# Optimization experiments

Hardware: AMD Instinct MI355X
Metric: run time of the kernel (lower is better)

The kernel has to match this reference:

```python
import jax, jax.numpy as jnp
import numpy as np

B, N, C, H = 32, 577, 768, 12
D = C // H  # head dim 64
HID = 3072  # hardcoded Mlp hidden
ALPHA = 0.1
EPS = 1e-6


def setup_inputs() -> dict:
    key = jax.random.key(0)
    ks = jax.random.split(key, 8)
    s = 0.02
    return {
        "x": jax.random.normal(ks[0], (B, N, C), jnp.float32),
        "attn_weight": jax.random.uniform(ks[1], (B, N - 1), jnp.float32),
        "ln1_w": jnp.ones((C,), jnp.float32),
        "ln1_b": jnp.zeros((C,), jnp.float32),
        "qkv_w": jax.random.normal(ks[2], (3 * C, C), jnp.float32) * s,
        "qkv_b": jnp.zeros((3 * C,), jnp.float32),
        "proj_w": jax.random.normal(ks[3], (C, C), jnp.float32) * s,
        "proj_b": jnp.zeros((C,), jnp.float32),
        "ln2_w": jnp.ones((C,), jnp.float32),
        "ln2_b": jnp.zeros((C,), jnp.float32),
        "fc1_w": jax.random.normal(ks[4], (HID, C), jnp.float32) * s,
        "fc1_b": jnp.zeros((HID,), jnp.float32),
        "fc2_w": jax.random.normal(ks[5], (C, HID), jnp.float32) * s,
        "fc2_b": jnp.zeros((C,), jnp.float32),
    }


def _ln(x, w, b):
    m = x.mean(-1, keepdims=True)
    v = jnp.var(x, axis=-1, keepdims=True)
    return (x - m) * jax.lax.rsqrt(v + EPS) * w + b


def reference(x, attn_weight, ln1_w, ln1_b, qkv_w, qkv_b, proj_w, proj_b,
              ln2_w, ln2_b, fc1_w, fc1_b, fc2_w, fc2_b):
    h = _ln(x, ln1_w, ln1_b)
    qkv = (h @ qkv_w.T + qkv_b).reshape(B, N, 3, H, D)
    q = qkv[:, :, 0].transpose(0, 2, 1, 3)  # [B,H,N,D]
    k = qkv[:, :, 1].transpose(0, 2, 1, 3)
    v = qkv[:, :, 2].transpose(0, 2, 1, 3)
    scale = D ** -0.5
    attn = jnp.einsum('bhnd,bhmd->bhnm', q, k) * scale  # [B,H,N,N]
    patch_attn = attn[:, :, 0, 1:]  # pre-reweight CLS->patch scores
    # multiplicative reweighting of CLS row (cols 1:) before softmax
    factor = jnp.concatenate(
        [jnp.ones((B, 1), attn.dtype), attn_weight * ALPHA + (1.0 - ALPHA)], axis=-1)
    attn = attn.at[:, :, 0, :].multiply(factor[:, None, :])
    attn = jax.nn.softmax(attn, axis=-1)
    out = jnp.einsum('bhnm,bhmd->bhnd', attn, v)
    out = out.transpose(0, 2, 1, 3).reshape(B, N, C)
    out = out @ proj_w.T + proj_b
    x = x + out
    h2 = _ln(x, ln2_w, ln2_b)
    h2 = jax.nn.gelu(h2 @ fc1_w.T + fc1_b, approximate=False)  # nn.GELU exact
    h2 = h2 @ fc2_w.T + fc2_b
    x = x + h2
    return (x, patch_attn)
```

## Files before the change

### kernel.cpp

```cpp
#include <hip/hip_runtime.h>
#include <hip/hip_bf16.h>
#include <cstdint>

#define BB 32
#define NN 577
#define CC 768
#define HH 12
#define HIDN 3072
#define MROWS (BB*NN)

typedef __attribute__((ext_vector_type(8))) short bf16x8;
typedef __attribute__((ext_vector_type(4))) float f32x4;

__device__ __forceinline__ float b2f(unsigned short u) {
    union { float f; unsigned int i; } x; x.i = ((unsigned int)u) << 16; return x.f;
}
__device__ __forceinline__ unsigned short f2b(float f) {
    union { float f; unsigned int i; } x; x.f = f;
    unsigned int i = x.i;
    i += 0x7fffu + ((i >> 16) & 1u);
    return (unsigned short)(i >> 16);
}

__device__ __forceinline__ void async16(const void* g, void* l) {
    __builtin_amdgcn_global_load_lds(
        (const __attribute__((address_space(1))) uint32_t*)g,
        (__attribute__((address_space(3))) uint32_t*)l, 16, 0, 0);
}

__device__ __forceinline__ float gelu_f(float v) {
    float ax = fabsf(v) * 0.70710678118654752f;
    float t = __builtin_amdgcn_rcpf(1.0f + 0.3275911f * ax);
    float poly = t * (0.254829592f + t * (-0.284496736f + t * (1.421413741f +
                 t * (-1.453152027f + t * 1.061405429f))));
    float e = __expf(-ax * ax);
    float erf_abs = 1.0f - poly * e;
    float erf_v = (v >= 0.f) ? erf_abs : -erf_abs;
    return 0.5f * v * (1.0f + erf_v);
}

__global__ void cvt4(const float* __restrict__ a, int na, unsigned short* __restrict__ oa,
                     const float* __restrict__ b, int nb, unsigned short* __restrict__ ob,
                     const float* __restrict__ c, int nc, unsigned short* __restrict__ oc,
                     const float* __restrict__ d, int nd, unsigned short* __restrict__ od) {
    int stride = gridDim.x * blockDim.x;
    int t = blockIdx.x * blockDim.x + threadIdx.x;
    for (int i = t; i < na; i += stride) oa[i] = f2b(a[i]);
    for (int i = t; i < nb; i += stride) ob[i] = f2b(b[i]);
    for (int i = t; i < nc; i += stride) oc[i] = f2b(c[i]);
    for (int i = t; i < nd; i += stride) od[i] = f2b(d[i]);
}

__global__ __launch_bounds__(256)
void ln_kernel(const float* __restrict__ x, const float* __restrict__ w,
               const float* __restrict__ bsv, unsigned short* __restrict__ out) {
    int row = blockIdx.x;
    const float* xr = x + (size_t)row * CC;
    float v[3]; float s = 0.f, ss = 0.f;
    #pragma unroll
    for (int i = 0; i < 3; ++i) {
        v[i] = xr[threadIdx.x + i * 256];
        s += v[i]; ss += v[i] * v[i];
    }
    int lane = threadIdx.x & 63, wv = threadIdx.x >> 6;
    #pragma unroll
    for (int off = 32; off; off >>= 1) { s += __shfl_down(s, off); ss += __shfl_down(ss, off); }
    __shared__ float rs[4], rss[4];
    __shared__ float mean_s, rstd_s;
    if (lane == 0) { rs[wv] = s; rss[wv] = ss; }
    __syncthreads();
    if (threadIdx.x == 0) {
        float S = rs[0] + rs[1] + rs[2] + rs[3];
        float SS = rss[0] + rss[1] + rss[2] + rss[3];
        float m = S * (1.0f / 768.0f);
        float var = SS * (1.0f / 768.0f) - m * m;
        mean_s = m; rstd_s = rsqrtf(var + 1e-6f);
    }
    __syncthreads();
    float m = mean_s, r = rstd_s;
    #pragma unroll
    for (int i = 0; i < 3; ++i) {
        int c = threadIdx.x + i * 256;
        out[(size_t)row * CC + c] = f2b((v[i] - m) * r * w[c] + bsv[c]);
    }
}

template <int EPI>
__global__ __launch_bounds__(256, 4)
void gemm_bt(const unsigned short* __restrict__ A, const unsigned short* __restrict__ Bw,
             const float* __restrict__ bias, const float* __restrict__ resid,
             unsigned short* __restrict__ outb, float* __restrict__ outf,
             int M, int N, int K) {
    const int NT = gridDim.x;
    const int MT = (M + 127) >> 7;
    int flat = blockIdx.y * NT + blockIdx.x;
    int xcd = flat & 7, s = flat >> 3;
    int n_t = s % NT, mj = s / NT;
    int m_t = xcd + 8 * mj;
    if (m_t >= MT) return;
    const int m0 = m_t * 128, n0 = n_t * 128;

    __shared__ __align__(16) unsigned short As[2][128 * 32];
    __shared__ __align__(16) unsigned short Bs[2][128 * 32];
    const int tid = threadIdx.x;
    const int wave = tid >> 6, lane = tid & 63;
    const int wr = wave >> 1, wc = wave & 1;
    const int quad = lane >> 4, l16 = lane & 15;

    f32x4 acc[4][4] = {};

    const int c0 = tid, c1 = 256 + tid;
    const int row0 = c0 >> 2, seg0 = c0 & 3;
    const int row1 = c1 >> 2, seg1 = c1 & 3;
    int gm0 = m0 + row0; if (gm0 > M - 1) gm0 = M - 1;
    int gm1 = m0 + row1; if (gm1 > M - 1) gm1 = M - 1;
    const unsigned short* a0 = A + (size_t)gm0 * K + seg0 * 8;
    const unsigned short* a1 = A + (size_t)gm1 * K + seg1 * 8;
    const unsigned short* b0 = Bw + (size_t)(n0 + row0) * K + seg0 * 8;
    const unsigned short* b1 = Bw + (size_t)(n0 + row1) * K + seg1 * 8;

    for (int k0 = 0; k0 < K; k0 += 64) {
        #pragma unroll
        for (int p = 0; p < 2; ++p) {
            int kk = k0 + p * 32;
            async16(a0 + kk, &As[p][c0 * 8]);
            async16(a1 + kk, &As[p][c1 * 8]);
            async16(b0 + kk, &Bs[p][c0 * 8]);
            async16(b1 + kk, &Bs[p][c1 * 8]);
        }
        __syncthreads();
        #pragma unroll
        for (int p = 0; p < 2; ++p) {
            bf16x8 bfr[4];
            #pragma unroll
            for (int ni = 0; ni < 4; ++ni)
                bfr[ni] = *(const bf16x8*)&Bs[p][(wc * 64 + ni * 16 + l16) * 32 + quad * 8];
            #pragma unroll
            for (int mi = 0; mi < 4; ++mi) {
                bf16x8 af = *(const bf16x8*)&As[p][(wr * 64 + mi * 16 + l16) * 32 + quad * 8];
                #pragma unroll
                for (int ni = 0; ni < 4; ++ni)
                    acc[mi][ni] = __builtin_amdgcn_mfma_f32_16x16x32_bf16(af, bfr[ni], acc[mi][ni], 0, 0, 0);
            }
        }
        __syncthreads();
    }

    #pragma unroll
    for (int mi = 0; mi < 4; ++mi) {
        #pragma unroll
        for (int r = 0; r < 4; ++r) {
            int grow = m0 + wr * 64 + mi * 16 + quad * 4 + r;
            if (grow >= M) continue;
            #pragma unroll
            for (int ni = 0; ni < 4; ++ni) {
                int gcol = n0 + wc * 64 + ni * 16 + l16;
                float v = acc[mi][ni][r] + bias[gcol];
                size_t idx = (size_t)grow * N + gcol;
                if (EPI == 0) {
                    outb[idx] = f2b(v);
                } else if (EPI == 1) {
                    outb[idx] = f2b(gelu_f(v));
                } else {
                    outf[idx] = resid[idx] + v;
                }
            }
        }
    }
}

__global__ __launch_bounds__(256)
void attn_mfma(const unsigned short* __restrict__ qkv, const float* __restrict__ aw,
               unsigned short* __restrict__ O, float* __restrict__ patch) {
    const int qt = blockIdx.x, h = blockIdx.y, b = blockIdx.z;
    const int tid = threadIdx.x, wv = tid >> 6, lane = tid & 63;
    const int quad = lane >> 4, l16 = lane & 15;

    __shared__ __align__(16) unsigned short Ks[64 * 72];
    __shared__ __align__(16) unsigned short Vt[64 * 72];
    __shared__ __align__(16) unsigned short Pt[4][16 * 72];

    int qrow = qt * 64 + wv * 16 + l16;
    int qclamp = qrow < NN ? qrow : NN - 1;
    const unsigned short* qbase = qkv + (size_t)(b * NN + qclamp) * 2304 + h * 64;
    bf16x8 qf[2];
    qf[0] = *(const bf16x8*)(qbase + quad * 8);
    qf[1] = *(const bf16x8*)(qbase + 32 + quad * 8);
    #pragma unroll
    for (int i = 0; i < 2; ++i) {
        union { bf16x8 v; unsigned short u[8]; } t; t.v = qf[i];
        #pragma unroll
        for (int j = 0; j < 8; ++j) t.u[j] = f2b(b2f(t.u[j]) * 0.125f);
        qf[i] = t.v;
    }

    union { bf16x8 v; unsigned short u[8]; } onesf;
    #pragma unroll
    for (int j = 0; j < 8; ++j) onesf.u[j] = (l16 == 0) ? (unsigned short)0x3F80 : (unsigned short)0;

    f32x4 o[4] = {};
    f32x4 o5 = {};
    float mst[4];
    #pragma unroll
    for (int r = 0; r < 4; ++r) mst[r] = -1.0e30f;

    int keyc[2], segc[2], swzc[2];
    const unsigned short* kb_base;
    const unsigned short* vb_base;
    {
        int c0 = tid, c1 = 256 + tid;
        keyc[0] = c0 >> 3; segc[0] = c0 & 7;
        keyc[1] = c1 >> 3; segc[1] = c1 & 7;
        #pragma unroll
        for (int i = 0; i < 2; ++i) {
            int kg = keyc[i] >> 3, kl = keyc[i] & 7;
            swzc[i] = (kg ^ segc[i]) * 8 + kl;
        }
        kb_base = qkv + (size_t)b * NN * 2304 + 768 + h * 64;
        vb_base = qkv + (size_t)b * NN * 2304 + 1536 + h * 64;
    }

    bf16x8 pk[2], pv[2];
    #pragma unroll
    for (int i = 0; i < 2; ++i) {
        int gk = keyc[i]; if (gk >= NN) gk = NN - 1;
        pk[i] = *(const bf16x8*)(kb_base + (size_t)gk * 2304 + segc[i] * 8);
        pv[i] = *(const bf16x8*)(vb_base + (size_t)gk * 2304 + segc[i] * 8);
    }

    for (int kt = 0; kt < 10; ++kt) {
        __syncthreads();
        #pragma unroll
        for (int i = 0; i < 2; ++i) {
            *(bf16x8*)&Ks[keyc[i] * 72 + segc[i] * 8] = pk[i];
            union { bf16x8 v; unsigned short u[8]; } t; t.v = pv[i];
            #pragma unroll
            for (int e = 0; e < 8; ++e)
                Vt[(segc[i] * 8 + e) * 72 + swzc[i]] = t.u[e];
        }
        __syncthreads();

        if (kt < 9) {
            #pragma unroll
            for (int i = 0; i < 2; ++i) {
                int gk = (kt + 1) * 64 + keyc[i]; if (gk >= NN) gk = NN - 1;
                pk[i] = *(const bf16x8*)(kb_base + (size_t)gk * 2304 + segc[i] * 8);
                pv[i] = *(const bf16x8*)(vb_base + (size_t)gk * 2304 + segc[i] * 8);
            }
        }

        f32x4 s[4];
        __builtin_amdgcn_s_setprio(1);
        #pragma unroll
        for (int ni = 0; ni < 4; ++ni) {
            bf16x8 b0 = *(const bf16x8*)&Ks[(ni * 16 + l16) * 72 + quad * 8];
            bf16x8 b1 = *(const bf16x8*)&Ks[(ni * 16 + l16) * 72 + 32 + quad * 8];
            f32x4 acc = {};
            acc = __builtin_amdgcn_mfma_f32_16x16x32_bf16(qf[0], b0, acc, 0, 0, 0);
            acc = __builtin_amdgcn_mfma_f32_16x16x32_bf16(qf[1], b1, acc, 0, 0, 0);
            s[ni] = acc;
        }
        __builtin_amdgcn_s_setprio(0);

        if (kt == 9) {
            #pragma unroll
            for (int ni = 0; ni < 4; ++ni) {
                if (ni * 16 + l16 != 0) {
                    #pragma unroll
                    for (int r = 0; r < 4; ++r) s[ni][r] = -1.0e30f;
                }
            }
        }

        if (qt == 0 && wv == 0 && quad == 0) {
            #pragma unroll
            for (int ni = 0; ni < 4; ++ni) {
                int gkey = kt * 64 + ni * 16 + l16;
                if (gkey >= 1 && gkey < NN) {
                    patch[(size_t)(b * HH + h) * (NN - 1) + gkey - 1] = s[ni][0];
                    float f = aw[b * (NN - 1) + gkey - 1] * 0.1f + 0.9f;
                    s[ni][0] *= f;
                }
            }
        }

        float al[4];
        #pragma unroll
        for (int r = 0; r < 4; ++r) {
            float tm = fmaxf(fmaxf(s[0][r], s[1][r]), fmaxf(s[2][r], s[3][r]));
            tm = fmaxf(tm, __shfl_xor(tm, 1));
            tm = fmaxf(tm, __shfl_xor(tm, 2));
            tm = fmaxf(tm, __shfl_xor(tm, 4));
            tm = fmaxf(tm, __shfl_xor(tm, 8));
            float nm = fmaxf(mst[r], tm);
            al[r] = __expf(mst[r] - nm);
            mst[r] = nm;
        }
        #pragma unroll
        for (int r = 0; r < 4; ++r) {
            #pragma unroll
            for (int ni = 0; ni < 4; ++ni) {
                float p = __expf(s[ni][r] - mst[r]);
                Pt[wv][(quad * 4 + r) * 72 + ni * 16 + l16] = f2b(p);
            }
            #pragma unroll
            for (int ni = 0; ni < 4; ++ni) o[ni][r] *= al[r];
            o5[r] *= al[r];
        }

        __builtin_amdgcn_s_setprio(1);
        #pragma unroll
        for (int kc = 0; kc < 2; ++kc) {
            bf16x8 af = *(const bf16x8*)&Pt[wv][l16 * 72 + kc * 32 + quad * 8];
            #pragma unroll
            for (int ni = 0; ni < 4; ++ni) {
                int d = ni * 16 + l16;
                int gs = (kc * 4 + quad) ^ (d >> 3);
                bf16x8 vf = *(const bf16x8*)&Vt[d * 72 + gs * 8];
                o[ni] = __builtin_amdgcn_mfma_f32_16x16x32_bf16(af, vf, o[ni], 0, 0, 0);
            }
            o5 = __builtin_amdgcn_mfma_f32_16x16x32_bf16(af, onesf.v, o5, 0, 0, 0);
        }
        __builtin_amdgcn_s_setprio(0);
    }

    #pragma unroll
    for (int r = 0; r < 4; ++r) {
        float lr = __shfl(o5[r], quad << 4);
        float inv = (lr > 0.f) ? __builtin_amdgcn_rcpf(lr) : 0.f;
        int row = qt * 64 + wv * 16 + quad * 4 + r;
        if (row < NN) {
            #pragma unroll
            for (int ni = 0; ni < 4; ++ni)
                O[(size_t)(b * NN + row) * CC + h * 64 + ni * 16 + l16] = f2b(o[ni][r] * inv);
        }
    }
}

extern "C" void kernel_launch(void* const* d_in, const int* in_sizes, int n_in,
                              void* d_out, int out_size, void* d_ws, size_t ws_size,
                              hipStream_t stream) {
    const float* x       = (const float*)d_in[0];
    const float* aw      = (const float*)d_in[1];
    const float* ln1w    = (const float*)d_in[2];
    const float* ln1b    = (const float*)d_in[3];
    const float* qkvw_f  = (const float*)d_in[4];
    const float* qkvb    = (const float*)d_in[5];
    const float* projw_f = (const float*)d_in[6];
    const float* projb   = (const float*)d_in[7];
    const float* ln2w    = (const float*)d_in[8];
    const float* ln2b    = (const float*)d_in[9];
    const float* fc1w_f  = (const float*)d_in[10];
    const float* fc1b    = (const float*)d_in[11];
    const float* fc2w_f  = (const float*)d_in[12];
    const float* fc2b    = (const float*)d_in[13];

    char* ws = (char*)d_ws;
    unsigned short* h_bf  = (unsigned short*)(ws + 0);
    unsigned short* qkv   = (unsigned short*)(ws + 28360704);
    unsigned short* g1    = (unsigned short*)(ws + 0);
    unsigned short* attno = (unsigned short*)(ws + 113442816);
    float*          x1    = (float*)(ws + 141803520);
    unsigned short* h2    = (unsigned short*)(ws + 198524928);
    unsigned short* qkvw  = (unsigned short*)(ws + 226885632);
    unsigned short* projw = (unsigned short*)(ws + 230424576);
    unsigned short* fc1w  = (unsigned short*)(ws + 231604224);
    unsigned short* fc2w  = (unsigned short*)(ws + 236322816);

    float* out_x = (float*)d_out;
    float* out_patch = out_x + (size_t)MROWS * CC;

    cvt4<<<1024, 256, 0, stream>>>(qkvw_f, 2304 * 768, qkvw,
                                   projw_f, 768 * 768, projw,
                                   fc1w_f, 3072 * 768, fc1w,
                                   fc2w_f, 768 * 3072, fc2w);
    ln_kernel<<<MROWS, 256, 0, stream>>>(x, ln1w, ln1b, h_bf);
    gemm_bt<0><<<dim3(18, 152), 256, 0, stream>>>(h_bf, qkvw, qkvb, nullptr, qkv, nullptr,
                                                  MROWS, 2304, 768);
    attn_mfma<<<dim3(10, HH, BB), 256, 0, stream>>>(qkv, aw, attno, out_patch);
    gemm_bt<2><<<dim3(6, 152), 256, 0, stream>>>(attno, projw, projb, x, nullptr, x1,
                                                 MROWS, 768, 768);
    ln_kernel<<<MROWS, 256, 0, stream>>>(x1, ln2w, ln2b, h2);
    gemm_bt<1><<<dim3(24, 152), 256, 0, stream>>>(h2, fc1w, fc1b, nullptr, g1, nullptr,
                                                  MROWS, 3072, 768);
    gemm_bt<2><<<dim3(6, 152), 256, 0, stream>>>(g1, fc2w, fc2b, x1, nullptr, out_x,
                                                 MROWS, 768, 3072);
}
```

Baseline: 682.7 us.

## Software-pipeline GEMM K loop with rolling double-buffered async loads

Replaces the load-all-then-compute K loop with a rolling two-stage pipeline. The next 32-wide K slice is issued into the buffer just consumed, and partial vmcnt waits let global-to-LDS copies overlap MFMA work. The goal is to hide global memory latency that was previously exposed at every 64-wide step. It relies on hand-placed s_waitcnt and raw barriers, which risks ordering bugs if the compiler reorders LDS reads or the async16 count assumption is wrong.

Result: slower. 710.8 us (+4.1%).

```diff
diff --git a/kernel.cpp b/kernel.cpp
--- a/kernel.cpp
+++ b/kernel.cpp
@@ -94,8 +94,8 @@
     const int NT = gridDim.x;
     const int MT = (M + 127) >> 7;
     int flat = blockIdx.y * NT + blockIdx.x;
-    int xcd = flat & 7, s = flat >> 3;
-    int n_t = s % NT, mj = s / NT;
+    int xcd = flat & 7, s0 = flat >> 3;
+    int n_t = s0 % NT, mj = s0 / NT;
     int m_t = xcd + 8 * mj;
     if (m_t >= MT) return;
     const int m0 = m_t * 128, n0 = n_t * 128;
@@ -119,31 +119,44 @@
     const unsigned short* b0 = Bw + (size_t)(n0 + row0) * K + seg0 * 8;
     const unsigned short* b1 = Bw + (size_t)(n0 + row1) * K + seg1 * 8;
 
-    for (int k0 = 0; k0 < K; k0 += 64) {
-        #pragma unroll
-        for (int p = 0; p < 2; ++p) {
-            int kk = k0 + p * 32;
-            async16(a0 + kk, &As[p][c0 * 8]);
-            async16(a1 + kk, &As[p][c1 * 8]);
-            async16(b0 + kk, &Bs[p][c0 * 8]);
-            async16(b1 + kk, &Bs[p][c1 * 8]);
-        }
-        __syncthreads();
-        #pragma unroll
-        for (int p = 0; p < 2; ++p) {
-            bf16x8 bfr[4];
+    const int S = K >> 5;
+
+    async16(a0 +  0, &As[0][c0 * 8]);
+    async16(a1 +  0, &As[0][c1 * 8]);
+    async16(b0 +  0, &Bs[0][c0 * 8]);
+    async16(b1 +  0, &Bs[0][c1 * 8]);
+    async16(a0 + 32, &As[1][c0 * 8]);
+    async16(a1 + 32, &As[1][c1 * 8]);
+    async16(b0 + 32, &Bs[1][c0 * 8]);
+    async16(b1 + 32, &Bs[1][c1 * 8]);
+    asm volatile("s_waitcnt vmcnt(4)" ::: "memory");
+    __builtin_amdgcn_s_barrier();
+
+    for (int s = 0; s < S; ++s) {
+        const int cur = s & 1;
+        bf16x8 bfr[4];
+        #pragma unroll
+        for (int ni = 0; ni < 4; ++ni)
+            bfr[ni] = *(const bf16x8*)&Bs[cur][(wc * 64 + ni * 16 + l16) * 32 + quad * 8];
+        #pragma unroll
+        for (int mi = 0; mi < 4; ++mi) {
+            bf16x8 af = *(const bf16x8*)&As[cur][(wr * 64 + mi * 16 + l16) * 32 + quad * 8];
             #pragma unroll
             for (int ni = 0; ni < 4; ++ni)
-                bfr[ni] = *(const bf16x8*)&Bs[p][(wc * 64 + ni * 16 + l16) * 32 + quad * 8];
-            #pragma unroll
-            for (int mi = 0; mi < 4; ++mi) {
-                bf16x8 af = *(const bf16x8*)&As[p][(wr * 64 + mi * 16 + l16) * 32 + quad * 8];
-                #pragma unroll
-                for (int ni = 0; ni < 4; ++ni)
-                    acc[mi][ni] = __builtin_amdgcn_mfma_f32_16x16x32_bf16(af, bfr[ni], acc[mi][ni], 0, 0, 0);
-            }
-        }
-        __syncthreads();
+                acc[mi][ni] = __builtin_amdgcn_mfma_f32_16x16x32_bf16(af, bfr[ni], acc[mi][ni], 0, 0, 0);
+        }
+        __builtin_amdgcn_s_barrier();
+        if (s + 2 < S) {
+            const int kk = (s + 2) << 5;
+            async16(a0 + kk, &As[cur][c0 * 8]);
+            async16(a1 + kk, &As[cur][c1 * 8]);
+            async16(b0 + kk, &Bs[cur][c0 * 8]);
+            async16(b1 + kk, &Bs[cur][c1 * 8]);
+            asm volatile("s_waitcnt vmcnt(4)" ::: "memory");
+        } else {
+            asm volatile("s_waitcnt vmcnt(0)" ::: "memory");
+        }
+        __builtin_amdgcn_s_barrier();
     }
 
     #pragma unroll
```
